# Performance work log

Measured on AMD Instinct MI355X. Metric: run time of the kernel, lower is better.

Reference implementation:

```python
import jax, jax.numpy as jnp
import numpy as np

N = 50000      # nodes per type
E = 1600000    # edges per edge type
D = 128        # feature / hidden dim
OUT = 2


def setup_inputs() -> dict:
    key = jax.random.key(0)
    ks = jax.random.split(key, 20)
    f = lambda k, shape, scale=0.05: jax.random.normal(k, shape, dtype=jnp.float32) * scale
    inp = {
        'x_student': jax.random.normal(ks[0], (N, D), dtype=jnp.float32),
        'x_studies': jax.random.normal(ks[1], (N, D), dtype=jnp.float32),
        'ei_s2st': jax.random.randint(ks[2], (2, E), 0, N, dtype=jnp.int64),
        'ei_st2s': jax.random.randint(ks[3], (2, E), 0, N, dtype=jnp.int64),
        'l1_st_Wl': f(ks[4], (D, D)), 'l1_st_b': f(ks[5], (D,)), 'l1_st_Wr': f(ks[6], (D, D)),
        'l1_s_Wl': f(ks[7], (D, D)), 'l1_s_b': f(ks[8], (D,)), 'l1_s_Wr': f(ks[9], (D, D)),
        'l2_st_Wl': f(ks[10], (D, D)), 'l2_st_b': f(ks[11], (D,)), 'l2_st_Wr': f(ks[12], (D, D)),
        'l2_s_Wl': f(ks[13], (D, D)), 'l2_s_b': f(ks[14], (D,)), 'l2_s_Wr': f(ks[15], (D, D)),
        'lin_W': f(ks[16], (D, OUT)), 'lin_b': f(ks[17], (OUT,)),
    }
    return inp


def _sage(x_src, x_dst, ei, Wl, b, Wr, n_dst):
    # PyG SAGEConv, aggr='mean': lin_l(mean_{j in N(i)} x_j) + lin_r(x_i)
    src, dst = ei[0], ei[1]
    msg = x_src[src]                                              # [E, D] gather
    s = jax.ops.segment_sum(msg, dst, num_segments=n_dst)         # [n_dst, D]
    cnt = jax.ops.segment_sum(jnp.ones((ei.shape[1],), x_src.dtype), dst, num_segments=n_dst)
    mean = s / jnp.maximum(cnt, 1.0)[:, None]                     # isolated nodes -> 0
    return mean @ Wl + b + x_dst @ Wr


def reference(x_student, x_studies, ei_s2st, ei_st2s,
              l1_st_Wl, l1_st_b, l1_st_Wr, l1_s_Wl, l1_s_b, l1_s_Wr,
              l2_st_Wl, l2_st_b, l2_st_Wr, l2_s_Wl, l2_s_b, l2_s_Wr,
              lin_W, lin_b):
    # layer 1 (each dst type receives from exactly one edge type)
    h_st = _sage(x_student, x_studies, ei_s2st, l1_st_Wl, l1_st_b, l1_st_Wr, N)
    h_s = _sage(x_studies, x_student, ei_st2s, l1_s_Wl, l1_s_b, l1_s_Wr, N)
    h_st = jax.nn.relu(h_st)
    h_s = jax.nn.relu(h_s)
    # layer 2
    h_st2 = _sage(h_s, h_st, ei_s2st, l2_st_Wl, l2_st_b, l2_st_Wr, N)
    # final linear on 'studies' node type
    return h_st2 @ lin_W + lin_b
```

## Files before the change

### kernel.cpp

```cpp
#include <hip/hip_runtime.h>

#define NN 50000
#define DD 128
#define EE 1600000
#define NBUK 196

typedef unsigned int uint;
typedef unsigned short ushort;
typedef __attribute__((ext_vector_type(8))) short bf16x8;
typedef __attribute__((ext_vector_type(4))) float f32x4;

__device__ __forceinline__ ushort f2bf(float f) {
    uint u = __float_as_uint(f);
    u += 0x7fffu + ((u >> 16) & 1u);
    return (ushort)(u >> 16);
}

__global__ void __launch_bounds__(256) f32_to_bf16_kernel(const float* __restrict__ in,
                                                          ushort* __restrict__ out, int n4) {
    int i = blockIdx.x * blockDim.x + threadIdx.x;
    if (i < n4) {
        float4 v = ((const float4*)in)[i];
        ushort4 o;
        o.x = f2bf(v.x);
        o.y = f2bf(v.y);
        o.z = f2bf(v.z);
        o.w = f2bf(v.w);
        ((ushort4*)out)[i] = o;
    }
}

__global__ void __launch_bounds__(256) wconv_kernel(const float* __restrict__ w,
                                                    ushort* __restrict__ wt) {
    int idx = blockIdx.x * 256 + threadIdx.x;
    int c = idx >> 7, k = idx & 127;
    wt[idx] = f2bf(w[k * DD + c]);
}


__global__ void __launch_bounds__(1024) bucket_hist_kernel(const int* __restrict__ dst,
                                                           int* __restrict__ bcnt) {
    __shared__ int h[NBUK];
    int t = threadIdx.x;
    for (int i = t; i < NBUK; i += 1024) h[i] = 0;
    __syncthreads();
    for (int e = blockIdx.x * 1024 + t; e < EE; e += gridDim.x * 1024)
        atomicAdd(&h[dst[e] >> 8], 1);
    __syncthreads();
    for (int i = t; i < NBUK; i += 1024)
        if (h[i]) atomicAdd(&bcnt[i], h[i]);
}

__global__ void __launch_bounds__(256) bucket_scan_kernel(const int* __restrict__ bcnt,
                                                          int* __restrict__ bbase,
                                                          int* __restrict__ bcur) {
    int t = threadIdx.x, lane = t & 63, w = t >> 6;
    int v = bcnt[t];
    int inc = v;
#pragma unroll
    for (int off = 1; off < 64; off <<= 1) {
        int n = __shfl_up(inc, off);
        if (lane >= off) inc += n;
    }
    __shared__ int wsum[4];
    if (lane == 63) wsum[w] = inc;
    __syncthreads();
    int woff = 0;
#pragma unroll
    for (int i = 0; i < 4; ++i)
        if (i < w) woff += wsum[i];
    int ex = woff + inc - v;
    bbase[t] = ex;
    bcur[t] = ex;
}

__global__ void __launch_bounds__(1024) bucket_scatter_kernel(const int* __restrict__ src,
                                                              const int* __restrict__ dst,
                                                              int* __restrict__ bcur,
                                                              uint* __restrict__ packed) {
    __shared__ int cnt[NBUK];
    __shared__ int base[NBUK];
    int t = threadIdx.x;
    long e0 = (long)blockIdx.x * 4096;
    for (int i = t; i < NBUK; i += 1024) cnt[i] = 0;
    __syncthreads();
    int b[4], off[4];
    uint pk[4];
#pragma unroll
    for (int u = 0; u < 4; ++u) {
        long e = e0 + u * 1024 + t;
        if (e < EE) {
            int d = dst[e];
            int s = src[e];
            b[u] = d >> 8;
            pk[u] = (uint)s | ((uint)(d & 255) << 16);
            off[u] = atomicAdd(&cnt[b[u]], 1);
        } else {
            b[u] = -1;
        }
    }
    __syncthreads();
    for (int i = t; i < NBUK; i += 1024) base[i] = cnt[i] ? atomicAdd(&bcur[i], cnt[i]) : 0;
    __syncthreads();
#pragma unroll
    for (int u = 0; u < 4; ++u)
        if (b[u] >= 0) packed[base[b[u]] + off[u]] = pk[u];
}

__global__ void __launch_bounds__(1024) bucket_build_kernel(const uint* __restrict__ packed,
                                                            const int* __restrict__ bbase,
                                                            const int* __restrict__ bcnt,
                                                            int* __restrict__ rowptr,
                                                            ushort* __restrict__ sorted) {
    int b = blockIdx.x;
    int t = threadIdx.x;
    int ebeg = bbase[b], ecnt = bcnt[b];
    int node0 = b << 8;
    int nn = min(256, NN - node0);
    __shared__ int deg[256];
    __shared__ int cur[256];
    __shared__ int wsum[4];
    for (int i = t; i < 256; i += 1024) deg[i] = 0;
    __syncthreads();
    for (int i = t; i < ecnt; i += 1024) {
        uint p = packed[ebeg + i];
        atomicAdd(&deg[(p >> 16) & 255], 1);
    }
    __syncthreads();
    int lane = t & 63, w = t >> 6;
    int v = (t < 256) ? deg[t] : 0;
    int inc = v;
#pragma unroll
    for (int off = 1; off < 64; off <<= 1) {
        int n = __shfl_up(inc, off);
        if (lane >= off) inc += n;
    }
    if (t < 256 && lane == 63) wsum[w] = inc;
    __syncthreads();
    if (t < 256) {
        int woff = 0;
#pragma unroll
        for (int i = 0; i < 4; ++i)
            if (i < w) woff += wsum[i];
        int ex = woff + inc - v;
        if (t < nn) rowptr[node0 + t] = ebeg + ex;
        cur[t] = ebeg + ex;
    }
    if (b == NBUK - 1 && t == 0) rowptr[NN] = ebeg + ecnt;
    __syncthreads();
    for (int i = t; i < ecnt; i += 1024) {
        uint p = packed[ebeg + i];
        int pos = atomicAdd(&cur[(p >> 16) & 255], 1);
        sorted[pos] = (ushort)(p & 0xFFFFu);
    }
}

__global__ void __launch_bounds__(256) agg_kernel(const uint* __restrict__ xu,
                                                  const int* __restrict__ rowptr,
                                                  const ushort* __restrict__ srcs,
                                                  uint* __restrict__ out) {
    int wid = (blockIdx.x * blockDim.x + threadIdx.x) >> 6;
    int lane = threadIdx.x & 63;
    if (wid >= NN) return;
    int beg = rowptr[wid], end = rowptr[wid + 1];
    float ax = 0.f, ay = 0.f;
    int j = beg;
    int nfull = (end - beg) >> 3;
    int ss[8];
    if (nfull > 0) {
#pragma unroll
        for (int u = 0; u < 8; ++u) ss[u] = (int)srcs[j + u];
    }
    for (int ch = 0; ch < nfull; ++ch) {
        uint vv[8];
#pragma unroll
        for (int u = 0; u < 8; ++u) vv[u] = xu[ss[u] * 64 + lane];
        int base = j + 8;
        bool more = (ch + 1 < nfull);
        int sn[8];
#pragma unroll
        for (int u = 0; u < 8; ++u) sn[u] = more ? (int)srcs[base + u] : 0;
#pragma unroll
        for (int u = 0; u < 8; ++u) {
            ax += __uint_as_float(vv[u] << 16);
            ay += __uint_as_float(vv[u] & 0xffff0000u);
        }
#pragma unroll
        for (int u = 0; u < 8; ++u) ss[u] = sn[u];
        j += 8;
    }
    for (; j < end; ++j) {
        int s = (int)srcs[j];
        uint v = xu[s * 64 + lane];
        ax += __uint_as_float(v << 16);
        ay += __uint_as_float(v & 0xffff0000u);
    }
    float inv = (end > beg) ? 1.0f / (float)(end - beg) : 0.0f;
    uint lo = (uint)f2bf(ax * inv);
    uint hi = (uint)f2bf(ay * inv);
    out[(size_t)wid * 64 + lane] = lo | (hi << 16);
}

template <int MODE>
__global__ void __launch_bounds__(256) mfma_gemm_kernel(
    const ushort* __restrict__ A1, const ushort* __restrict__ Wt1,
    const ushort* __restrict__ A2, const ushort* __restrict__ Wt2,
    const float* __restrict__ bias, const float* __restrict__ Wf,
    const float* __restrict__ bf, void* __restrict__ out) {
    int t = threadIdx.x;
    int wave = t >> 6, l = t & 63;
    int row0 = blockIdx.x * 64 + wave * 16;
    int lr = l & 15;
    int kq = l >> 4;

    f32x4 acc[8];
#pragma unroll
    for (int i = 0; i < 8; ++i) acc[i] = (f32x4){0.f, 0.f, 0.f, 0.f};

    int arow = row0 + lr;
    int safe = (arow < NN) ? arow : 0;
    const ushort* a1p = A1 + (size_t)safe * DD + kq * 8;
    const ushort* a2p = A2 + (size_t)safe * DD + kq * 8;

#pragma unroll
    for (int ks = 0; ks < 4; ++ks) {
        bf16x8 a1 = *(const bf16x8*)(a1p + ks * 32);
        bf16x8 a2 = *(const bf16x8*)(a2p + ks * 32);
#pragma unroll
        for (int ct = 0; ct < 8; ++ct) {
            bf16x8 b1 = *(const bf16x8*)(Wt1 + (size_t)(ct * 16 + lr) * DD + ks * 32 + kq * 8);
            acc[ct] = __builtin_amdgcn_mfma_f32_16x16x32_bf16(a1, b1, acc[ct], 0, 0, 0);
            bf16x8 b2 = *(const bf16x8*)(Wt2 + (size_t)(ct * 16 + lr) * DD + ks * 32 + kq * 8);
            acc[ct] = __builtin_amdgcn_mfma_f32_16x16x32_bf16(a2, b2, acc[ct], 0, 0, 0);
        }
    }

    if (MODE == 1) {
        int crow = row0 + kq * 4;
#pragma unroll
        for (int ct = 0; ct < 8; ++ct) {
            float b = bias[ct * 16 + lr];
#pragma unroll
            for (int r = 0; r < 4; ++r) {
                int rr = crow + r;
                if (rr < NN) {
                    float v = fmaxf(acc[ct][r] + b, 0.f);
                    ((ushort*)out)[(size_t)rr * DD + ct * 16 + lr] = f2bf(v);
                }
            }
        }
    } else {
        float s[4][2] = {{0.f, 0.f}, {0.f, 0.f}, {0.f, 0.f}, {0.f, 0.f}};
#pragma unroll
        for (int ct = 0; ct < 8; ++ct) {
            int c = ct * 16 + lr;
            float b = bias[c];
            float wf0 = Wf[c * 2 + 0], wf1 = Wf[c * 2 + 1];
#pragma unroll
            for (int r = 0; r < 4; ++r) {
                float v = acc[ct][r] + b;
                s[r][0] += v * wf0;
                s[r][1] += v * wf1;
            }
        }
#pragma unroll
        for (int m = 1; m < 16; m <<= 1) {
#pragma unroll
            for (int r = 0; r < 4; ++r) {
                s[r][0] += __shfl_xor(s[r][0], m);
                s[r][1] += __shfl_xor(s[r][1], m);
            }
        }
        if (lr == 0) {
            int crow = row0 + kq * 4;
#pragma unroll
            for (int r = 0; r < 4; ++r) {
                int rr = crow + r;
                if (rr < NN) {
                    ((float*)out)[(size_t)rr * 2 + 0] = s[r][0] + bf[0];
                    ((float*)out)[(size_t)rr * 2 + 1] = s[r][1] + bf[1];
                }
            }
        }
    }
}

extern "C" void kernel_launch(void* const* d_in, const int* in_sizes, int n_in,
                              void* d_out, int out_size, void* d_ws, size_t ws_size,
                              hipStream_t stream) {
    const float* x_student = (const float*)d_in[0];
    const float* x_studies = (const float*)d_in[1];
    const int* ei_s2st = (const int*)d_in[2];
    const int* ei_st2s = (const int*)d_in[3];
    const float* l1_st_Wl = (const float*)d_in[4];
    const float* l1_st_b = (const float*)d_in[5];
    const float* l1_st_Wr = (const float*)d_in[6];
    const float* l1_s_Wl = (const float*)d_in[7];
    const float* l1_s_b = (const float*)d_in[8];
    const float* l1_s_Wr = (const float*)d_in[9];
    const float* l2_st_Wl = (const float*)d_in[10];
    const float* l2_st_b = (const float*)d_in[11];
    const float* l2_st_Wr = (const float*)d_in[12];
    const float* lin_W = (const float*)d_in[16];
    const float* lin_b = (const float*)d_in[17];
    float* out = (float*)d_out;

    char* ws = (char*)d_ws;
    ushort* aggbuf = (ushort*)ws;
    ushort* hst_bf = aggbuf + (size_t)NN * DD;
    ushort* hs_bf = hst_bf + (size_t)NN * DD;
    ushort* xstu_bf = hs_bf + (size_t)NN * DD;
    ushort* xsts_bf = xstu_bf + (size_t)NN * DD;
    ushort* Wt = xsts_bf + (size_t)NN * DD;
    uint* packed = (uint*)(Wt + 6 * DD * DD);
    int* rowptr_a = (int*)(packed + EE);
    int* rowptr_b = rowptr_a + (NN + 1);
    int* bcnt_a = rowptr_b + (NN + 1);
    int* bcnt_b = bcnt_a + 256;
    int* bbase_a = bcnt_b + 256;
    int* bcur_a = bbase_a + 256;
    int* bbase_b = bcur_a + 256;
    int* bcur_b = bbase_b + 256;
    ushort* sorted_a = (ushort*)(bcur_b + 256);
    ushort* sorted_b = sorted_a + EE;

    const int* src_a = ei_s2st;
    const int* dst_a = ei_s2st + EE;
    const int* src_b = ei_st2s;
    const int* dst_b = ei_st2s + EE;

    const int cvGrid = (NN * DD / 4 + 255) / 256;
    const int scGrid = (EE + 4095) / 4096;
    const int aggGrid = (NN * 64 + 255) / 256;
    const int gemmGrid = (NN + 63) / 64;

    f32_to_bf16_kernel<<<cvGrid, 256, 0, stream>>>(x_student, xstu_bf, NN * DD / 4);
    f32_to_bf16_kernel<<<cvGrid, 256, 0, stream>>>(x_studies, xsts_bf, NN * DD / 4);
    wconv_kernel<<<64, 256, 0, stream>>>(l1_st_Wl, Wt + 0 * DD * DD);
    wconv_kernel<<<64, 256, 0, stream>>>(l1_st_Wr, Wt + 1 * DD * DD);
    wconv_kernel<<<64, 256, 0, stream>>>(l1_s_Wl, Wt + 2 * DD * DD);
    wconv_kernel<<<64, 256, 0, stream>>>(l1_s_Wr, Wt + 3 * DD * DD);
    wconv_kernel<<<64, 256, 0, stream>>>(l2_st_Wl, Wt + 4 * DD * DD);
    wconv_kernel<<<64, 256, 0, stream>>>(l2_st_Wr, Wt + 5 * DD * DD);

    (void)hipMemsetAsync(bcnt_a, 0, 2 * 256 * sizeof(int), stream);
    bucket_hist_kernel<<<256, 1024, 0, stream>>>(dst_a, bcnt_a);
    bucket_hist_kernel<<<256, 1024, 0, stream>>>(dst_b, bcnt_b);
    bucket_scan_kernel<<<1, 256, 0, stream>>>(bcnt_a, bbase_a, bcur_a);
    bucket_scan_kernel<<<1, 256, 0, stream>>>(bcnt_b, bbase_b, bcur_b);
    bucket_scatter_kernel<<<scGrid, 1024, 0, stream>>>(src_a, dst_a, bcur_a, packed);
    bucket_build_kernel<<<NBUK, 1024, 0, stream>>>(packed, bbase_a, bcnt_a, rowptr_a, sorted_a);
    bucket_scatter_kernel<<<scGrid, 1024, 0, stream>>>(src_b, dst_b, bcur_b, packed);
    bucket_build_kernel<<<NBUK, 1024, 0, stream>>>(packed, bbase_b, bcnt_b, rowptr_b, sorted_b);

    agg_kernel<<<aggGrid, 256, 0, stream>>>((const uint*)xstu_bf, rowptr_a, sorted_a,
                                            (uint*)aggbuf);
    mfma_gemm_kernel<1><<<gemmGrid, 256, 0, stream>>>(aggbuf, Wt + 0 * DD * DD, xsts_bf,
                                                      Wt + 1 * DD * DD, l1_st_b, nullptr,
                                                      nullptr, hst_bf);
    agg_kernel<<<aggGrid, 256, 0, stream>>>((const uint*)xsts_bf, rowptr_b, sorted_b,
                                            (uint*)aggbuf);
    mfma_gemm_kernel<1><<<gemmGrid, 256, 0, stream>>>(aggbuf, Wt + 2 * DD * DD, xstu_bf,
                                                      Wt + 3 * DD * DD, l1_s_b, nullptr,
                                                      nullptr, hs_bf);

    agg_kernel<<<aggGrid, 256, 0, stream>>>((const uint*)hs_bf, rowptr_a, sorted_a,
                                            (uint*)aggbuf);
    mfma_gemm_kernel<2><<<gemmGrid, 256, 0, stream>>>(aggbuf, Wt + 4 * DD * DD, hst_bf,
                                                      Wt + 5 * DD * DD, l2_st_b, lin_W, lin_b,
                                                      out);
}
```

Baseline: 504.4 us.

## Sort CSR neighbors by source range and batch small setup kernels

The bucket build now keys each edge by destination node and the high bits of its source index, so each node's neighbor list comes out ordered by source region. This is meant to improve cache locality of the feature gathers in the aggregation kernels. Separately, the two feature conversions, six weight conversions, two histograms and two scans are merged into single launches to cut launch overhead. The build kernel uses more shared memory and does a longer scan, which adds cost to preprocessing.

```diff
diff --git a/kernel.cpp b/kernel.cpp
--- a/kernel.cpp
+++ b/kernel.cpp
@@ -4,6 +4,8 @@
 #define DD 128
 #define EE 1600000
 #define NBUK 196
+#define NR 13
+#define NKEY (256 * NR)
 
 typedef unsigned int uint;
 typedef unsigned short ushort;
@@ -16,9 +18,15 @@
     return (ushort)(u >> 16);
 }
 
-__global__ void __launch_bounds__(256) f32_to_bf16_kernel(const float* __restrict__ in,
-                                                          ushort* __restrict__ out, int n4) {
-    int i = blockIdx.x * blockDim.x + threadIdx.x;
+__global__ void __launch_bounds__(256) f32_to_bf16_kernel(const float* __restrict__ in0,
+                                                          ushort* __restrict__ out0,
+                                                          const float* __restrict__ in1,
+                                                          ushort* __restrict__ out1, int n4) {
+    int half = gridDim.x >> 1;
+    const float* in = (blockIdx.x < half) ? in0 : in1;
+    ushort* out = (blockIdx.x < half) ? out0 : out1;
+    int bid = (blockIdx.x < half) ? blockIdx.x : blockIdx.x - half;
+    int i = bid * 256 + threadIdx.x;
     if (i < n4) {
         float4 v = ((const float4*)in)[i];
         ushort4 o;
@@ -30,30 +38,56 @@
     }
 }
 
-__global__ void __launch_bounds__(256) wconv_kernel(const float* __restrict__ w,
-                                                    ushort* __restrict__ wt) {
-    int idx = blockIdx.x * 256 + threadIdx.x;
+__global__ void __launch_bounds__(256) wconv6_kernel(const float* __restrict__ w0,
+                                                     const float* __restrict__ w1,
+                                                     const float* __restrict__ w2,
+                                                     const float* __restrict__ w3,
+                                                     const float* __restrict__ w4,
+                                                     const float* __restrict__ w5,
+                                                     ushort* __restrict__ wt) {
+    int m = blockIdx.x >> 6;
+    const float* w;
+    switch (m) {
+        case 0: w = w0; break;
+        case 1: w = w1; break;
+        case 2: w = w2; break;
+        case 3: w = w3; break;
+        case 4: w = w4; break;
+        default: w = w5; break;
+    }
+    int idx = (blockIdx.x & 63) * 256 + threadIdx.x;
     int c = idx >> 7, k = idx & 127;
-    wt[idx] = f2bf(w[k * DD + c]);
-}
-
-
-__global__ void __launch_bounds__(1024) bucket_hist_kernel(const int* __restrict__ dst,
-                                                           int* __restrict__ bcnt) {
+    wt[m * DD * DD + idx] = f2bf(w[k * DD + c]);
+}
+
+
+__global__ void __launch_bounds__(1024) bucket_hist_kernel(const int* __restrict__ dstA,
+                                                           int* __restrict__ bcntA,
+                                                           const int* __restrict__ dstB,
+                                                           int* __restrict__ bcntB) {
+    int half = gridDim.x >> 1;
+    const int* dst = (blockIdx.x < half) ? dstA : dstB;
+    int* bcnt = (blockIdx.x < half) ? bcntA : bcntB;
+    int bid = (blockIdx.x < half) ? blockIdx.x : blockIdx.x - half;
     __shared__ int h[NBUK];
     int t = threadIdx.x;
     for (int i = t; i < NBUK; i += 1024) h[i] = 0;
     __syncthreads();
-    for (int e = blockIdx.x * 1024 + t; e < EE; e += gridDim.x * 1024)
-        atomicAdd(&h[dst[e] >> 8], 1);
+    for (int e = bid * 1024 + t; e < EE; e += half * 1024) atomicAdd(&h[dst[e] >> 8], 1);
     __syncthreads();
     for (int i = t; i < NBUK; i += 1024)
         if (h[i]) atomicAdd(&bcnt[i], h[i]);
 }
 
-__global__ void __launch_bounds__(256) bucket_scan_kernel(const int* __restrict__ bcnt,
-                                                          int* __restrict__ bbase,
-                                                          int* __restrict__ bcur) {
+__global__ void __launch_bounds__(256) bucket_scan_kernel(const int* __restrict__ bcntA,
+                                                          int* __restrict__ bbaseA,
+                                                          int* __restrict__ bcurA,
+                                                          const int* __restrict__ bcntB,
+                                                          int* __restrict__ bbaseB,
+                                                          int* __restrict__ bcurB) {
+    const int* bcnt = (blockIdx.x == 0) ? bcntA : bcntB;
+    int* bbase = (blockIdx.x == 0) ? bbaseA : bbaseB;
+    int* bcur = (blockIdx.x == 0) ? bcurA : bcurB;
     int t = threadIdx.x, lane = t & 63, w = t >> 6;
     int v = bcnt[t];
     int inc = v;
@@ -117,41 +151,53 @@
     int ebeg = bbase[b], ecnt = bcnt[b];
     int node0 = b << 8;
     int nn = min(256, NN - node0);
-    __shared__ int deg[256];
-    __shared__ int cur[256];
-    __shared__ int wsum[4];
-    for (int i = t; i < 256; i += 1024) deg[i] = 0;
+    __shared__ int deg[NKEY];
+    __shared__ int cur[NKEY];
+    __shared__ int wsum[16];
+    for (int i = t; i < NKEY; i += 1024) deg[i] = 0;
     __syncthreads();
     for (int i = t; i < ecnt; i += 1024) {
         uint p = packed[ebeg + i];
-        atomicAdd(&deg[(p >> 16) & 255], 1);
-    }
-    __syncthreads();
+        int key = (int)((p >> 16) & 255) * NR + (int)((p & 0xFFFFu) >> 12);
+        atomicAdd(&deg[key], 1);
+    }
+    __syncthreads();
+    int base4 = t * 4;
+    int local[4];
+    int s = 0;
+#pragma unroll
+    for (int k = 0; k < 4; ++k) {
+        int v = (base4 + k < NKEY) ? deg[base4 + k] : 0;
+        local[k] = s;
+        s += v;
+    }
     int lane = t & 63, w = t >> 6;
-    int v = (t < 256) ? deg[t] : 0;
-    int inc = v;
+    int inc = s;
 #pragma unroll
     for (int off = 1; off < 64; off <<= 1) {
         int n = __shfl_up(inc, off);
         if (lane >= off) inc += n;
     }
-    if (t < 256 && lane == 63) wsum[w] = inc;
-    __syncthreads();
-    if (t < 256) {
-        int woff = 0;
-#pragma unroll
-        for (int i = 0; i < 4; ++i)
-            if (i < w) woff += wsum[i];
-        int ex = woff + inc - v;
-        if (t < nn) rowptr[node0 + t] = ebeg + ex;
-        cur[t] = ebeg + ex;
-    }
+    if (lane == 63) wsum[w] = inc;
+    __syncthreads();
+    int woff = 0;
+#pragma unroll
+    for (int i = 0; i < 16; ++i)
+        if (i < w) woff += wsum[i];
+    int te = woff + inc - s;
+#pragma unroll
+    for (int k = 0; k < 4; ++k)
+        if (base4 + k < NKEY) cur[base4 + k] = ebeg + te + local[k];
+    __syncthreads();
+    if (t < nn) rowptr[node0 + t] = cur[t * NR];
     if (b == NBUK - 1 && t == 0) rowptr[NN] = ebeg + ecnt;
     __syncthreads();
     for (int i = t; i < ecnt; i += 1024) {
         uint p = packed[ebeg + i];
-        int pos = atomicAdd(&cur[(p >> 16) & 255], 1);
-        sorted[pos] = (ushort)(p & 0xFFFFu);
+        int sv = (int)(p & 0xFFFFu);
+        int key = (int)((p >> 16) & 255) * NR + (sv >> 12);
+        int pos = atomicAdd(&cur[key], 1);
+        sorted[pos] = (ushort)sv;
     }
 }
 
@@ -334,20 +380,14 @@
     const int aggGrid = (NN * 64 + 255) / 256;
     const int gemmGrid = (NN + 63) / 64;
 
-    f32_to_bf16_kernel<<<cvGrid, 256, 0, stream>>>(x_student, xstu_bf, NN * DD / 4);
-    f32_to_bf16_kernel<<<cvGrid, 256, 0, stream>>>(x_studies, xsts_bf, NN * DD / 4);
-    wconv_kernel<<<64, 256, 0, stream>>>(l1_st_Wl, Wt + 0 * DD * DD);
-    wconv_kernel<<<64, 256, 0, stream>>>(l1_st_Wr, Wt + 1 * DD * DD);
-    wconv_kernel<<<64, 256, 0, stream>>>(l1_s_Wl, Wt + 2 * DD * DD);
-    wconv_kernel<<<64, 256, 0, stream>>>(l1_s_Wr, Wt + 3 * DD * DD);
-    wconv_kernel<<<64, 256, 0, stream>>>(l2_st_Wl, Wt + 4 * DD * DD);
-    wconv_kernel<<<64, 256, 0, stream>>>(l2_st_Wr, Wt + 5 * DD * DD);
+    f32_to_bf16_kernel<<<2 * cvGrid, 256, 0, stream>>>(x_student, xstu_bf, x_studies, xsts_bf,
+                                                       NN * DD / 4);
+    wconv6_kernel<<<6 * 64, 256, 0, stream>>>(l1_st_Wl, l1_st_Wr, l1_s_Wl, l1_s_Wr, l2_st_Wl,
+                                              l2_st_Wr, Wt);
 
     (void)hipMemsetAsync(bcnt_a, 0, 2 * 256 * sizeof(int), stream);
-    bucket_hist_kernel<<<256, 1024, 0, stream>>>(dst_a, bcnt_a);
-    bucket_hist_kernel<<<256, 1024, 0, stream>>>(dst_b, bcnt_b);
-    bucket_scan_kernel<<<1, 256, 0, stream>>>(bcnt_a, bbase_a, bcur_a);
-    bucket_scan_kernel<<<1, 256, 0, stream>>>(bcnt_b, bbase_b, bcur_b);
+    bucket_hist_kernel<<<512, 1024, 0, stream>>>(dst_a, bcnt_a, dst_b, bcnt_b);
+    bucket_scan_kernel<<<2, 256, 0, stream>>>(bcnt_a, bbase_a, bcur_a, bcnt_b, bbase_b, bcur_b);
     bucket_scatter_kernel<<<scGrid, 1024, 0, stream>>>(src_a, dst_a, bcur_a, packed);
     bucket_build_kernel<<<NBUK, 1024, 0, stream>>>(packed, bbase_a, bcnt_a, rowptr_a, sorted_a);
     bucket_scatter_kernel<<<scGrid, 1024, 0, stream>>>(src_b, dst_b, bcur_b, packed);
```

New measurement: 483.2 us. 4.2% less time.
